# Performance work log

Measured on AMD Instinct MI355X. Metric: run time of the kernel, lower is better.

The kernel has to match this reference:

```python
import jax, jax.numpy as jnp
import numpy as np

H = 32        # num_attention_heads
KVH = 8       # num_key_value_heads
D = 2048      # hidden_size
HD = D // H   # head_dim = 64
GROUPS = H // KVH


def setup_inputs() -> dict:
    key = jax.random.key(0)
    k1, k2, k3, k4 = jax.random.split(key, 4)
    B, T = 2, 2048
    x = jax.random.normal(k1, (B, T, D), dtype=jnp.float32)
    wq = jax.random.normal(k2, (D, H * HD), dtype=jnp.float32) * (D ** -0.5)
    wkv = jax.random.normal(k3, (D, 2 * KVH * HD), dtype=jnp.float32) * (D ** -0.5)
    wo = jax.random.normal(k4, (H * HD, D), dtype=jnp.float32) * (D ** -0.5)
    return {"x": x, "wq": wq, "wkv": wkv, "wo": wo}


def reference(x, wq, wkv, wo):
    B, T, _ = x.shape
    scale = HD ** -0.5
    # projections
    q = (x @ wq).reshape(B, T, H, HD).transpose(0, 2, 1, 3)        # [B,H,T,hd]
    kv = x @ wkv                                                    # [B,T,2*KVH*hd]
    k, v = jnp.split(kv, 2, axis=-1)
    k = k.reshape(B, T, KVH, HD).transpose(0, 2, 1, 3)              # [B,KVH,T,hd]
    v = v.reshape(B, T, KVH, HD).transpose(0, 2, 1, 3)
    # repeat_interleave KV heads to match Q heads
    k = jnp.repeat(k, GROUPS, axis=1)                               # [B,H,T,hd]
    v = jnp.repeat(v, GROUPS, axis=1)
    scores = jnp.einsum('bhqd,bhkd->bhqk', q, k) * scale            # [B,H,T,T]
    causal = jnp.triu(jnp.ones((T, T), dtype=bool), k=1)
    scores = jnp.where(causal, -jnp.inf, scores)
    attn = jax.nn.softmax(scores, axis=-1)
    out = jnp.einsum('bhqk,bhkd->bhqd', attn, v)                    # [B,H,T,hd]
    out = out.transpose(0, 2, 1, 3).reshape(B, T, H * HD)
    return out @ wo
```

## Files before the change

kernel.cpp:

```cpp
#include <hip/hip_runtime.h>

using bf16   = __bf16;
using bf16x8 = __attribute__((ext_vector_type(8))) __bf16;
using f32x4  = __attribute__((ext_vector_type(4))) float;
using u32x4  = __attribute__((ext_vector_type(4))) unsigned;

#define T_SEQ 2048
#define NQKV 3072

__device__ __forceinline__ void async_cp16(const bf16* g, bf16* l) {
  __builtin_amdgcn_global_load_lds((__attribute__((address_space(1))) void*)(void*)g,
                                   (__attribute__((address_space(3))) void*)l, 16, 0, 0);
}

__global__ __launch_bounds__(256) void prep_kernel(
    const float* __restrict__ x, bf16* __restrict__ xbf,
    const float* __restrict__ wq, const float* __restrict__ wkv,
    const float* __restrict__ wo, bf16* __restrict__ w1,
    bf16* __restrict__ woT) {
  const int z = blockIdx.z;
  if (z == 0) {
    long i = (((long)blockIdx.y * 64 + blockIdx.x) * 256 + threadIdx.x) * 8;
    float4 a = *(const float4*)(x + i);
    float4 c = *(const float4*)(x + i + 4);
    bf16x8 v;
    v[0] = (bf16)a.x; v[1] = (bf16)a.y; v[2] = (bf16)a.z; v[3] = (bf16)a.w;
    v[4] = (bf16)c.x; v[5] = (bf16)c.y; v[6] = (bf16)c.z; v[7] = (bf16)c.w;
    *(bf16x8*)(xbf + i) = v;
    return;
  }
  const float* in; bf16* out; int R, C;
  if (z == 1)      { in = wq;  out = w1;                R = 2048; C = 2048; }
  else if (z == 2) { if (blockIdx.x >= 32) return;
                     in = wkv; out = w1 + 2048L * 2048; R = 2048; C = 1024; }
  else             { in = wo;  out = woT;               R = 2048; C = 2048; }
  __shared__ float tile[32][33];
  const int tc = blockIdx.x * 32;
  const int tr = blockIdx.y * 32;
  const int t = threadIdx.x;
  const int lr = t >> 5;
  const int lc = t & 31;
#pragma unroll
  for (int i = 0; i < 4; ++i)
    tile[lr + i * 8][lc] = in[(size_t)(tr + lr + i * 8) * C + tc + lc];
  __syncthreads();
#pragma unroll
  for (int i = 0; i < 4; ++i)
    out[(size_t)(tc + lr + i * 8) * R + tr + lc] = (bf16)tile[lc][lr + i * 8];
}

__global__ __launch_bounds__(256) void transpose_cvt(const float* __restrict__ in,
                                                     bf16* __restrict__ out,
                                                     int R, int C) {
  __shared__ float tile[32][33];
  const int tc = blockIdx.x * 32;
  const int tr = blockIdx.y * 32;
  const int t = threadIdx.x;
  const int lr = t >> 5;
  const int lc = t & 31;
#pragma unroll
  for (int i = 0; i < 4; ++i)
    tile[lr + i * 8][lc] = in[(size_t)(tr + lr + i * 8) * C + tc + lc];
  __syncthreads();
#pragma unroll
  for (int i = 0; i < 4; ++i)
    out[(size_t)(tc + lr + i * 8) * R + tr + lc] = (bf16)tile[lc][lr + i * 8];
}

__global__ __launch_bounds__(256) void transpose_v(const bf16* __restrict__ in,
                                                   bf16* __restrict__ out) {
  __shared__ bf16 tile[32][33];
  const int c0 = blockIdx.x * 32;
  const int r0 = blockIdx.y * 32;
  const int t = threadIdx.x;
  const int lr = t >> 5;
  const int lc = t & 31;
#pragma unroll
  for (int i = 0; i < 4; ++i)
    tile[lr + i * 8][lc] = in[(size_t)(r0 + lr + i * 8) * NQKV + 2560 + c0 + lc];
  __syncthreads();
#pragma unroll
  for (int i = 0; i < 4; ++i) {
    int c = c0 + lr + i * 8;
    int r = r0 + lc;
    out[(size_t)((r >> 11) * 512 + c) * 2048 + (r & 2047)] = tile[lc][lr + i * 8];
  }
}

template <bool OUT_BF16, bool V_SPLIT>
__global__ __launch_bounds__(256, 4)
void gemm_kernel(const bf16* __restrict__ A, const bf16* __restrict__ Bt,
                 void* __restrict__ Cout, bf16* __restrict__ vTout,
                 int Kdim, int Ndim) {
  __shared__ __attribute__((aligned(16))) bf16 As[128 * 64];
  __shared__ __attribute__((aligned(16))) bf16 Bs[128 * 64];
  const int tid  = threadIdx.x;
  const int lane = tid & 63;
  const int wave = tid >> 6;
  const int l16  = lane & 15;
  const int q4   = lane >> 4;

  const int nwg = gridDim.x * gridDim.y;
  int wg = blockIdx.y * gridDim.x + blockIdx.x;
  if ((nwg & 7) == 0) wg = (wg & 7) * (nwg >> 3) + (wg >> 3);
  const long m0 = (long)(wg / gridDim.x) * 128;
  const long n0 = (long)(wg % gridDim.x) * 128;

  const int wm = (wave >> 1) * 64;
  const int wn = (wave & 1) * 64;

  f32x4 acc[4][4] = {};

  for (int k0 = 0; k0 < Kdim; k0 += 64) {
    __syncthreads();
#pragma unroll
    for (int rr = 0; rr < 4; ++rr) {
      int ci  = rr * 256 + tid;
      int row = ci >> 3;
      int chp = ci & 7;
      int ch  = chp ^ (row & 7);
      async_cp16(A + (m0 + row) * (long)Kdim + k0 + ch * 8, &As[ci * 8]);
      async_cp16(Bt + (n0 + row) * (long)Kdim + k0 + ch * 8, &Bs[ci * 8]);
    }
    __syncthreads();
#pragma unroll
    for (int ks = 0; ks < 2; ++ks) {
      bf16x8 af[4], bfr[4];
#pragma unroll
      for (int mt = 0; mt < 4; ++mt) {
        int row = wm + mt * 16 + l16;
        int chp = (ks * 4 + q4) ^ (row & 7);
        af[mt] = *(const bf16x8*)&As[row * 64 + chp * 8];
      }
#pragma unroll
      for (int nt = 0; nt < 4; ++nt) {
        int row = wn + nt * 16 + l16;
        int chp = (ks * 4 + q4) ^ (row & 7);
        bfr[nt] = *(const bf16x8*)&Bs[row * 64 + chp * 8];
      }
#pragma unroll
      for (int mt = 0; mt < 4; ++mt)
#pragma unroll
        for (int nt = 0; nt < 4; ++nt)
          acc[mt][nt] = __builtin_amdgcn_mfma_f32_16x16x32_bf16(af[mt], bfr[nt],
                                                                acc[mt][nt], 0, 0, 0);
    }
  }

  if constexpr (V_SPLIT) {
    if (n0 >= 2560) {
#pragma unroll
      for (int mt = 0; mt < 4; ++mt)
#pragma unroll
        for (int nt = 0; nt < 4; ++nt)
#pragma unroll
          for (int r = 0; r < 4; ++r) {
            long row = m0 + wm + mt * 16 + q4 * 4 + r;
            long c   = n0 + wn + nt * 16 + l16 - 2560;
            vTout[((row >> 11) * 512 + c) * 2048 + (row & 2047)] =
                (bf16)acc[mt][nt][r];
          }
      return;
    }
  }
#pragma unroll
  for (int mt = 0; mt < 4; ++mt)
#pragma unroll
    for (int nt = 0; nt < 4; ++nt)
#pragma unroll
      for (int r = 0; r < 4; ++r) {
        long row = m0 + wm + mt * 16 + q4 * 4 + r;
        long col = n0 + wn + nt * 16 + l16;
        float v = acc[mt][nt][r];
        if constexpr (OUT_BF16)
          ((bf16*)Cout)[row * Ndim + col] = (bf16)v;
        else
          ((float*)Cout)[row * Ndim + col] = v;
      }
}

__global__ __launch_bounds__(256, 3)
void attn_kernel(const bf16* __restrict__ qkv, const bf16* __restrict__ vT,
                 bf16* __restrict__ outb) {
  __shared__ __attribute__((aligned(16))) bf16 Ks[64 * 64];
  __shared__ __attribute__((aligned(16))) bf16 Vs[64 * 64];

  const int tid  = threadIdx.x;
  const int lane = tid & 63;
  const int wave = tid >> 6;
  const int l16  = lane & 15;
  const int q4   = lane >> 4;

  const int bid = blockIdx.x;
  const int qt  = 15 - (bid >> 6);
  const int bh  = bid & 63;
  const int b   = bh >> 5;
  const int h   = bh & 31;
  const int kvh = h >> 2;
  const long rowbase = (long)b * T_SEQ;

  const int qrow0 = qt * 128;
  const int wq0   = qrow0 + wave * 32;
  const float cexp = 0.125f * 1.4426950408889634f;

  bf16x8 aq[2][2];
#pragma unroll
  for (int mt = 0; mt < 2; ++mt)
#pragma unroll
    for (int ks = 0; ks < 2; ++ks) {
      bf16x8 v = *(const bf16x8*)(qkv +
          (rowbase + wq0 + mt * 16 + l16) * (long)NQKV + h * 64 + ks * 32 + q4 * 8);
#pragma unroll
      for (int i = 0; i < 8; ++i) v[i] = (bf16)((float)v[i] * cexp);
      aq[mt][ks] = v;
    }

  bf16x8 ones_f;
#pragma unroll
  for (int i = 0; i < 8; ++i) ones_f[i] = (l16 == 0) ? (bf16)1.0f : (bf16)0.0f;

  f32x4 o[2][4] = {};
  f32x4 o_l[2] = {};

  const bf16* kbase = qkv + rowbase * (long)NQKV + 2048 + kvh * 64;
  const bf16* vbase = vT + ((long)b * 512 + kvh * 64) * 2048;

  const int ntiles = (qrow0 + 128) >> 6;

  bf16x8 kr[2], vr[2];
#pragma unroll
  for (int h2 = 0; h2 < 2; ++h2) {
    int ci = h2 * 256 + tid, row = ci >> 3, ch = (ci & 7) ^ (row & 7);
    kr[h2] = *(const bf16x8*)(kbase + (long)row * NQKV + ch * 8);
    vr[h2] = *(const bf16x8*)(vbase + (long)row * 2048 + ch * 8);
  }

  for (int t = 0; t < ntiles; ++t) {
    const int j0 = t * 64;
    __syncthreads();
#pragma unroll
    for (int h2 = 0; h2 < 2; ++h2) {
      int ci = h2 * 256 + tid;
      *(bf16x8*)&Ks[ci * 8] = kr[h2];
      *(bf16x8*)&Vs[ci * 8] = vr[h2];
    }
    __syncthreads();
    if (t + 1 < ntiles) {
      const int jn = j0 + 64;
#pragma unroll
      for (int h2 = 0; h2 < 2; ++h2) {
        int ci = h2 * 256 + tid, row = ci >> 3, ch = (ci & 7) ^ (row & 7);
        kr[h2] = *(const bf16x8*)(kbase + (long)(jn + row) * NQKV + ch * 8);
        vr[h2] = *(const bf16x8*)(vbase + (long)row * 2048 + jn + ch * 8);
      }
    }
    if (j0 > wq0 + 31) continue;

    f32x4 s[2][4] = {};
#pragma unroll
    for (int ks = 0; ks < 2; ++ks) {
      bf16x8 bk[4];
#pragma unroll
      for (int nt = 0; nt < 4; ++nt) {
        int row  = nt * 16 + l16;
        int slot = (ks * 4 + q4) ^ (row & 7);
        bk[nt] = *(const bf16x8*)&Ks[row * 64 + slot * 8];
      }
#pragma unroll
      for (int mt = 0; mt < 2; ++mt)
#pragma unroll
        for (int nt = 0; nt < 4; ++nt)
          s[mt][nt] = __builtin_amdgcn_mfma_f32_16x16x32_bf16(bk[nt], aq[mt][ks],
                                                              s[mt][nt], 0, 0, 0);
    }

    if (j0 + 63 > wq0) {
#pragma unroll
      for (int mt = 0; mt < 2; ++mt)
#pragma unroll
        for (int nt = 0; nt < 4; ++nt)
#pragma unroll
          for (int r = 0; r < 4; ++r) {
            int rg = wq0 + mt * 16 + l16;
            int cg = j0 + nt * 16 + q4 * 4 + r;
            if (cg > rg) s[mt][nt][r] = -__builtin_inff();
          }
    }

    bf16x8 ap[2][2];
#pragma unroll
    for (int mt = 0; mt < 2; ++mt) {
      unsigned pk0, pk1, pk2, pk3, pk4, pk5, pk6, pk7;
      {
        float p0 = __builtin_amdgcn_exp2f(s[mt][0][0]);
        float p1 = __builtin_amdgcn_exp2f(s[mt][0][1]);
        float p2 = __builtin_amdgcn_exp2f(s[mt][0][2]);
        float p3 = __builtin_amdgcn_exp2f(s[mt][0][3]);
        asm("v_cvt_pk_bf16_f32 %0, %1, %2" : "=v"(pk0) : "v"(p0), "v"(p1));
        asm("v_cvt_pk_bf16_f32 %0, %1, %2" : "=v"(pk1) : "v"(p2), "v"(p3));
      }
      {
        float p0 = __builtin_amdgcn_exp2f(s[mt][1][0]);
        float p1 = __builtin_amdgcn_exp2f(s[mt][1][1]);
        float p2 = __builtin_amdgcn_exp2f(s[mt][1][2]);
        float p3 = __builtin_amdgcn_exp2f(s[mt][1][3]);
        asm("v_cvt_pk_bf16_f32 %0, %1, %2" : "=v"(pk2) : "v"(p0), "v"(p1));
        asm("v_cvt_pk_bf16_f32 %0, %1, %2" : "=v"(pk3) : "v"(p2), "v"(p3));
      }
      {
        float p0 = __builtin_amdgcn_exp2f(s[mt][2][0]);
        float p1 = __builtin_amdgcn_exp2f(s[mt][2][1]);
        float p2 = __builtin_amdgcn_exp2f(s[mt][2][2]);
        float p3 = __builtin_amdgcn_exp2f(s[mt][2][3]);
        asm("v_cvt_pk_bf16_f32 %0, %1, %2" : "=v"(pk4) : "v"(p0), "v"(p1));
        asm("v_cvt_pk_bf16_f32 %0, %1, %2" : "=v"(pk5) : "v"(p2), "v"(p3));
      }
      {
        float p0 = __builtin_amdgcn_exp2f(s[mt][3][0]);
        float p1 = __builtin_amdgcn_exp2f(s[mt][3][1]);
        float p2 = __builtin_amdgcn_exp2f(s[mt][3][2]);
        float p3 = __builtin_amdgcn_exp2f(s[mt][3][3]);
        asm("v_cvt_pk_bf16_f32 %0, %1, %2" : "=v"(pk6) : "v"(p0), "v"(p1));
        asm("v_cvt_pk_bf16_f32 %0, %1, %2" : "=v"(pk7) : "v"(p2), "v"(p3));
      }
      {
        unsigned a0 = pk0, b0 = pk2;
        asm("v_permlane32_swap_b32 %0, %1" : "+v"(a0), "+v"(b0));
        asm("v_permlane16_swap_b32 %0, %1" : "+v"(a0), "+v"(b0));
        unsigned a1 = pk1, b1 = pk3;
        asm("v_permlane32_swap_b32 %0, %1" : "+v"(a1), "+v"(b1));
        asm("v_permlane16_swap_b32 %0, %1" : "+v"(a1), "+v"(b1));
        u32x4 w; w.x = a0; w.y = a1; w.z = b0; w.w = b1;
        ap[mt][0] = __builtin_bit_cast(bf16x8, w);
      }
      {
        unsigned a0 = pk4, b0 = pk6;
        asm("v_permlane32_swap_b32 %0, %1" : "+v"(a0), "+v"(b0));
        asm("v_permlane16_swap_b32 %0, %1" : "+v"(a0), "+v"(b0));
        unsigned a1 = pk5, b1 = pk7;
        asm("v_permlane32_swap_b32 %0, %1" : "+v"(a1), "+v"(b1));
        asm("v_permlane16_swap_b32 %0, %1" : "+v"(a1), "+v"(b1));
        u32x4 w; w.x = a0; w.y = a1; w.z = b0; w.w = b1;
        ap[mt][1] = __builtin_bit_cast(bf16x8, w);
      }
    }

#pragma unroll
    for (int ks = 0; ks < 2; ++ks) {
      bf16x8 bv[4];
#pragma unroll
      for (int dt = 0; dt < 4; ++dt) {
        int row  = dt * 16 + l16;
        int slot = (ks * 4 + q4) ^ (row & 7);
        bv[dt] = *(const bf16x8*)&Vs[row * 64 + slot * 8];
      }
#pragma unroll
      for (int mt = 0; mt < 2; ++mt) {
#pragma unroll
        for (int dt = 0; dt < 4; ++dt)
          o[mt][dt] = __builtin_amdgcn_mfma_f32_16x16x32_bf16(ap[mt][ks], bv[dt],
                                                              o[mt][dt], 0, 0, 0);
        o_l[mt] = __builtin_amdgcn_mfma_f32_16x16x32_bf16(ap[mt][ks], ones_f,
                                                          o_l[mt], 0, 0, 0);
      }
    }
  }

#pragma unroll
  for (int mt = 0; mt < 2; ++mt) {
    float inv[4];
#pragma unroll
    for (int r = 0; r < 4; ++r) {
      float lsum = __shfl(o_l[mt][r], lane & 48);
      inv[r] = 1.0f / lsum;
    }
#pragma unroll
    for (int dt = 0; dt < 4; ++dt)
#pragma unroll
      for (int r = 0; r < 4; ++r) {
        long row = rowbase + wq0 + mt * 16 + q4 * 4 + r;
        int col = h * 64 + dt * 16 + l16;
        outb[row * 2048 + col] = (bf16)(o[mt][dt][r] * inv[r]);
      }
  }
}

extern "C" void kernel_launch(void* const* d_in, const int* in_sizes, int n_in,
                              void* d_out, int out_size, void* d_ws, size_t ws_size,
                              hipStream_t stream) {
  const float* x   = (const float*)d_in[0];
  const float* wq  = (const float*)d_in[1];
  const float* wkv = (const float*)d_in[2];
  const float* wo  = (const float*)d_in[3];
  float* out = (float*)d_out;
  char* ws = (char*)d_ws;

  bf16* xbf  = (bf16*)(ws + 0);
  bf16* w1   = (bf16*)(ws + 16777216);
  bf16* qkv  = (bf16*)(ws + 29360128);
  bf16* attn = xbf;

  const bool fused_v  = ws_size >= 67108864u;
  const bool woT_early = ws_size >= 62914560u;

  bf16* woT = woT_early ? (bf16*)(ws + 54525952) : qkv;
  bf16* vT  = fused_v   ? (bf16*)(ws + 62914560) : w1;

  prep_kernel<<<dim3(64, 64, woT_early ? 4 : 3), 256, 0, stream>>>(
      x, xbf, wq, wkv, wo, w1, woT);

  if (fused_v) {
    gemm_kernel<true, true><<<dim3(24, 32), 256, 0, stream>>>(
        xbf, w1, (void*)qkv, vT, 2048, 3072);
  } else {
    gemm_kernel<true, false><<<dim3(24, 32), 256, 0, stream>>>(
        xbf, w1, (void*)qkv, nullptr, 2048, 3072);
    transpose_v<<<dim3(16, 128), 256, 0, stream>>>(qkv, vT);
  }

  attn_kernel<<<1024, 256, 0, stream>>>(qkv, vT, attn);

  if (!woT_early)
    transpose_cvt<<<dim3(64, 64), 256, 0, stream>>>(wo, woT, 2048, 2048);

  gemm_kernel<false, false><<<dim3(16, 32), 256, 0, stream>>>(
      attn, woT, (void*)out, nullptr, 2048, 2048);
}
```

Measured before the change: 253.5 us.

## Use 256x256 eight-wave ping-pong GEMM for QKV projection

Adds a 512-thread GEMM kernel with 256x256 tiles and double-buffered LDS. It interleaves staged async global-to-LDS loads with four MFMA phases per K-step and raises wave priority during the MFMA bursts. The QKV projection now uses this kernel instead of the 128x128 version, aiming for more data reuse per tile and better overlap of loads with compute. The trade-offs are 192 workgroups on a large-CU GPU, which may leave some CUs idle, plus 128KB of LDS per block and higher register pressure.

```diff
diff --git a/kernel.cpp b/kernel.cpp
--- a/kernel.cpp
+++ b/kernel.cpp
@@ -87,6 +87,166 @@
   }
 }
 
+template <int KDIM, bool OUT_BF16, bool V_SPLIT>
+__global__ __launch_bounds__(512, 2)
+void gemm8p_kernel(const bf16* __restrict__ A, const bf16* __restrict__ Bt,
+                   void* __restrict__ Cout, bf16* __restrict__ vTout, int Ndim) {
+  constexpr int NT = KDIM / 64;
+  __shared__ __attribute__((aligned(16))) bf16 As[2][256 * 64];
+  __shared__ __attribute__((aligned(16))) bf16 Bs[2][256 * 64];
+
+  const int tid  = threadIdx.x;
+  const int lane = tid & 63;
+  const int wave = tid >> 6;
+  const int l16  = lane & 15;
+  const int q4   = lane >> 4;
+  const int wm   = (wave >> 2) * 128;
+  const int wn   = (wave & 3) * 64;
+
+  const int nwg = gridDim.x * gridDim.y;
+  int wg = blockIdx.y * gridDim.x + blockIdx.x;
+  wg = (wg & 7) * (nwg >> 3) + (wg >> 3);
+  const long m0 = (long)(wg / gridDim.x) * 256;
+  const long n0 = (long)(wg % gridDim.x) * 256;
+
+  const bf16* Ag = A + m0 * (long)KDIM;
+  const bf16* Bg = Bt + n0 * (long)KDIM;
+
+  f32x4 acc[8][4] = {};
+
+  auto stageAq = [&](int buf, int kt, int q) {
+    const long k0 = (long)kt * 64;
+    int row = q * 64 + (tid >> 3);
+    int ch  = (tid & 7) ^ (row & 7);
+    async_cp16(Ag + (long)row * KDIM + k0 + ch * 8,
+               &As[buf][row * 64 + (tid & 7) * 8]);
+  };
+  auto stageBq = [&](int buf, int kt, int q) {
+    const long k0 = (long)kt * 64;
+    int row = q * 64 + (tid >> 3);
+    int ch  = (tid & 7) ^ (row & 7);
+    async_cp16(Bg + (long)row * KDIM + k0 + ch * 8,
+               &Bs[buf][row * 64 + (tid & 7) * 8]);
+  };
+
+#pragma unroll
+  for (int q = 0; q < 4; ++q) stageAq(0, 0, q);
+#pragma unroll
+  for (int q = 0; q < 4; ++q) stageBq(0, 0, q);
+  stageAq(1, 1, 0);
+  stageAq(1, 1, 2);
+
+  bf16x8 aF[4], bF[4];
+
+  for (int t = 0; t < NT; ++t) {
+    const int cur = t & 1, nxt = cur ^ 1;
+    asm volatile("s_waitcnt vmcnt(2)" ::: "memory");
+    __builtin_amdgcn_s_barrier();
+
+#pragma unroll
+    for (int mt = 0; mt < 4; ++mt) {
+      int row = wm + mt * 16 + l16;
+      aF[mt] = *(const bf16x8*)&As[cur][row * 64 + (q4 ^ (row & 7)) * 8];
+    }
+#pragma unroll
+    for (int nt = 0; nt < 4; ++nt) {
+      int row = wn + nt * 16 + l16;
+      bF[nt] = *(const bf16x8*)&Bs[cur][row * 64 + (q4 ^ (row & 7)) * 8];
+    }
+    if (t + 1 < NT) { stageAq(nxt, t + 1, 1); stageAq(nxt, t + 1, 3); }
+    __builtin_amdgcn_s_barrier();
+    asm volatile("s_waitcnt lgkmcnt(0)" ::: "memory");
+    __builtin_amdgcn_s_setprio(1);
+#pragma unroll
+    for (int mt = 0; mt < 4; ++mt)
+#pragma unroll
+      for (int nt = 0; nt < 4; ++nt)
+        acc[mt][nt] = __builtin_amdgcn_mfma_f32_16x16x32_bf16(aF[mt], bF[nt],
+                                                              acc[mt][nt], 0, 0, 0);
+    __builtin_amdgcn_s_setprio(0);
+    __builtin_amdgcn_s_barrier();
+
+#pragma unroll
+    for (int mt = 0; mt < 4; ++mt) {
+      int row = wm + 64 + mt * 16 + l16;
+      aF[mt] = *(const bf16x8*)&As[cur][row * 64 + (q4 ^ (row & 7)) * 8];
+    }
+    if (t + 1 < NT) { stageBq(nxt, t + 1, 0); stageBq(nxt, t + 1, 1); }
+    __builtin_amdgcn_s_barrier();
+    asm volatile("s_waitcnt lgkmcnt(0)" ::: "memory");
+    __builtin_amdgcn_s_setprio(1);
+#pragma unroll
+    for (int mt = 0; mt < 4; ++mt)
+#pragma unroll
+      for (int nt = 0; nt < 4; ++nt)
+        acc[4 + mt][nt] = __builtin_amdgcn_mfma_f32_16x16x32_bf16(aF[mt], bF[nt],
+                                                                  acc[4 + mt][nt], 0, 0, 0);
+    __builtin_amdgcn_s_setprio(0);
+    __builtin_amdgcn_s_barrier();
+
+#pragma unroll
+    for (int mt = 0; mt < 4; ++mt) {
+      int row = wm + mt * 16 + l16;
+      aF[mt] = *(const bf16x8*)&As[cur][row * 64 + ((4 + q4) ^ (row & 7)) * 8];
+    }
+#pragma unroll
+    for (int nt = 0; nt < 4; ++nt) {
+      int row = wn + nt * 16 + l16;
+      bF[nt] = *(const bf16x8*)&Bs[cur][row * 64 + ((4 + q4) ^ (row & 7)) * 8];
+    }
+    if (t + 1 < NT) { stageBq(nxt, t + 1, 2); stageBq(nxt, t + 1, 3); }
+    __builtin_amdgcn_s_barrier();
+    asm volatile("s_waitcnt lgkmcnt(0)" ::: "memory");
+    __builtin_amdgcn_s_setprio(1);
+#pragma unroll
+    for (int mt = 0; mt < 4; ++mt)
+#pragma unroll
+      for (int nt = 0; nt < 4; ++nt)
+        acc[mt][nt] = __builtin_amdgcn_mfma_f32_16x16x32_bf16(aF[mt], bF[nt],
+                                                              acc[mt][nt], 0, 0, 0);
+    __builtin_amdgcn_s_setprio(0);
+    __builtin_amdgcn_s_barrier();
+
+#pragma unroll
+    for (int mt = 0; mt < 4; ++mt) {
+      int row = wm + 64 + mt * 16 + l16;
+      aF[mt] = *(const bf16x8*)&As[cur][row * 64 + ((4 + q4) ^ (row & 7)) * 8];
+    }
+    if (t + 2 < NT) { stageAq(cur, t + 2, 0); stageAq(cur, t + 2, 2); }
+    __builtin_amdgcn_s_barrier();
+    asm volatile("s_waitcnt lgkmcnt(0)" ::: "memory");
+    __builtin_amdgcn_s_setprio(1);
+#pragma unroll
+    for (int mt = 0; mt < 4; ++mt)
+#pragma unroll
+      for (int nt = 0; nt < 4; ++nt)
+        acc[4 + mt][nt] = __builtin_amdgcn_mfma_f32_16x16x32_bf16(aF[mt], bF[nt],
+                                                                  acc[4 + mt][nt], 0, 0, 0);
+    __builtin_amdgcn_s_setprio(0);
+  }
+
+#pragma unroll
+  for (int idx = 0; idx < 8; ++idx) {
+    const int mtop = idx >> 2, mt = idx & 3;
+#pragma unroll
+    for (int nt = 0; nt < 4; ++nt)
+#pragma unroll
+      for (int r = 0; r < 4; ++r) {
+        long row = m0 + wm + mtop * 64 + mt * 16 + q4 * 4 + r;
+        long col = n0 + wn + nt * 16 + l16;
+        float v = acc[idx][nt][r];
+        if (V_SPLIT && n0 >= 2560) {
+          long c = col - 2560;
+          vTout[((row >> 11) * 512 + c) * 2048 + (row & 2047)] = (bf16)v;
+        } else if constexpr (OUT_BF16) {
+          ((bf16*)Cout)[row * Ndim + col] = (bf16)v;
+        } else {
+          ((float*)Cout)[row * Ndim + col] = v;
+        }
+      }
+  }
+}
+
 template <bool OUT_BF16, bool V_SPLIT>
 __global__ __launch_bounds__(256, 4)
 void gemm_kernel(const bf16* __restrict__ A, const bf16* __restrict__ Bt,
@@ -410,11 +570,11 @@
       x, xbf, wq, wkv, wo, w1, woT);
 
   if (fused_v) {
-    gemm_kernel<true, true><<<dim3(24, 32), 256, 0, stream>>>(
-        xbf, w1, (void*)qkv, vT, 2048, 3072);
+    gemm8p_kernel<2048, true, true><<<dim3(12, 16), 512, 0, stream>>>(
+        xbf, w1, (void*)qkv, vT, 3072);
   } else {
-    gemm_kernel<true, false><<<dim3(24, 32), 256, 0, stream>>>(
-        xbf, w1, (void*)qkv, nullptr, 2048, 3072);
+    gemm8p_kernel<2048, true, false><<<dim3(12, 16), 512, 0, stream>>>(
+        xbf, w1, (void*)qkv, nullptr, 3072);
     transpose_v<<<dim3(16, 128), 256, 0, stream>>>(qkv, vT);
   }
 
```

Measured after the change: 274.5 us. 1.08x slower.
